# Optimization experiments

Measured on AMD Instinct MI355X. Metric: run time of the kernel, lower is better.

## Reference

```python
import jax, jax.numpy as jnp
import numpy as np

N_NODES = 100_000
N_EDGES = 1_600_000
N_FEAT = 128
N_HID = 64
N_CLASS = 10
N_LAYERS = 3
N_GRAPHS = 1000


def _linear_init(key, fan_in, fan_out):
    kw, kb = jax.random.split(key)
    s = 1.0 / np.sqrt(fan_in)
    w = jax.random.uniform(kw, (fan_in, fan_out), minval=-s, maxval=s, dtype=jnp.float32)
    b = jax.random.uniform(kb, (fan_out,), minval=-s, maxval=s, dtype=jnp.float32)
    return w, b


def setup_inputs() -> dict:
    key = jax.random.key(0)
    ks = jax.random.split(key, 16)
    x = jax.random.normal(ks[0], (N_NODES, N_FEAT), dtype=jnp.float32)
    edge_index = jax.random.randint(ks[1], (2, N_EDGES), 0, N_NODES, dtype=jnp.int64)
    batch = jnp.sort(jax.random.randint(ks[2], (N_NODES,), 0, N_GRAPHS, dtype=jnp.int64))

    pre_w, pre_b = _linear_init(ks[3], N_FEAT, N_HID)
    w1s, b1s, w2s, b2s = [], [], [], []
    for l in range(N_LAYERS):
        w1, b1 = _linear_init(jax.random.fold_in(ks[4], 2 * l), N_HID, N_HID)
        w2, b2 = _linear_init(jax.random.fold_in(ks[4], 2 * l + 1), N_HID, N_HID)
        w1s.append(w1); b1s.append(b1); w2s.append(w2); b2s.append(b2)
    post_w, post_b = _linear_init(ks[5], N_HID, N_HID)
    ro_w, ro_b = _linear_init(ks[6], N_HID, N_CLASS)

    return {
        "x": x, "edge_index": edge_index, "batch": batch,
        "pre_w": pre_w, "pre_b": pre_b,
        "conv_w1": jnp.stack(w1s), "conv_b1": jnp.stack(b1s),
        "conv_w2": jnp.stack(w2s), "conv_b2": jnp.stack(b2s),
        "post_w": post_w, "post_b": post_b,
        "ro_w": ro_w, "ro_b": ro_b,
    }


def reference(x, edge_index, batch, pre_w, pre_b, conv_w1, conv_b1, conv_w2, conv_b2, post_w, post_b, ro_w, ro_b):
    src = edge_index[0]  # message source (x_j)
    dst = edge_index[1]  # message target

    h = x @ pre_w + pre_b  # [N, H]
    for l in range(N_LAYERS):
        # GINConv, eps=0: MLP((1+eps)*h_i + sum_{j in N(i)} h_j)
        agg = jax.ops.segment_sum(h[src], dst, num_segments=N_NODES)
        z = h + agg
        z = jax.nn.relu(z @ conv_w1[l] + conv_b1[l]) @ conv_w2[l] + conv_b2[l]
        h = jax.nn.relu(z)  # dropout is identity in eval mode

    g = jax.ops.segment_sum(h, batch, num_segments=N_GRAPHS)  # global_add_pool [G, H]
    g = jax.nn.relu(g @ post_w + post_b)
    logits = g @ ro_w + ro_b
    return jax.nn.log_softmax(logits, axis=1)
```

## Files before the change

kernel.cpp:

```cpp
#include <hip/hip_runtime.h>
#include <math.h>

#define N_NODES  100000
#define N_FEAT   128
#define N_HID    64
#define N_CLASS  10
#define N_GRAPHS 1000
#define N_EDGES  1600000
#define NTILES   1563
#define BLK_N    128
#define NT2      782
#define HF_PASS  8
#define HF_RANGE 12500
#define CSR_STRIDE 64
#define EMAX_LDS 32

__device__ __forceinline__ float bflo(unsigned u) { return __uint_as_float(u << 16); }
__device__ __forceinline__ float bfhi(unsigned u) { return __uint_as_float(u & 0xffff0000u); }
__device__ __forceinline__ unsigned bf_rne(float f) {
    unsigned u = __float_as_uint(f);
    return (u + 0x7fffu + ((u >> 16) & 1u)) >> 16;
}
__device__ __forceinline__ unsigned pack2(float a, float b) {
    return bf_rne(a) | (bf_rne(b) << 16);
}

__global__ __launch_bounds__(256, 4) void pre_kernel(
    const float* __restrict__ x, const float* __restrict__ W,
    const float* __restrict__ b, uint2* __restrict__ h)
{
    __shared__ float xs[64][68];
    __shared__ float ws[64][68];
    const int tid = threadIdx.x;
    const int tx = tid & 15, ty = tid >> 4;
    const int n0 = blockIdx.x * 64;

    float acc[4][4];
#pragma unroll
    for (int i = 0; i < 4; ++i)
#pragma unroll
        for (int j = 0; j < 4; ++j) acc[i][j] = 0.f;

    for (int p = 0; p < 2; ++p) {
        __syncthreads();
#pragma unroll
        for (int t = 0; t < 4; ++t) {
            const int idx = t * 256 + tid;
            const int m = idx >> 4, kv = idx & 15;
            float4 v = make_float4(0.f, 0.f, 0.f, 0.f);
            if (n0 + m < N_NODES)
                v = *(const float4*)(x + (size_t)(n0 + m) * N_FEAT + p * 64 + kv * 4);
            *(float4*)&xs[m][kv * 4] = v;
            *(float4*)&ws[m][kv * 4] =
                *(const float4*)(W + (size_t)(p * 64 + m) * N_HID + kv * 4);
        }
        __syncthreads();
#pragma unroll 2
        for (int k4 = 0; k4 < 16; ++k4) {
            float4 a[4], bb[4];
#pragma unroll
            for (int i = 0; i < 4; ++i)
                a[i] = *(const float4*)&xs[ty + 16 * i][k4 * 4];
#pragma unroll
            for (int j = 0; j < 4; ++j)
                bb[j] = *(const float4*)&ws[k4 * 4 + j][tx * 4];
#pragma unroll
            for (int i = 0; i < 4; ++i) {
                const float* ap = (const float*)&a[i];
#pragma unroll
                for (int j = 0; j < 4; ++j) {
                    const float* bp = (const float*)&bb[j];
#pragma unroll
                    for (int c = 0; c < 4; ++c)
                        acc[i][c] = fmaf(ap[j], bp[c], acc[i][c]);
                }
            }
        }
    }

    const float4 bias = *(const float4*)(b + tx * 4);
#pragma unroll
    for (int i = 0; i < 4; ++i) {
        const int node = n0 + ty + 16 * i;
        if (node < N_NODES) {
            h[(size_t)node * 16 + tx] = make_uint2(
                pack2(acc[i][0] + bias.x, acc[i][1] + bias.y),
                pack2(acc[i][2] + bias.z, acc[i][3] + bias.w));
        }
    }
}

__global__ __launch_bounds__(256) void hist_fill_kernel(
    const int* __restrict__ ei, int* __restrict__ deg, int* __restrict__ csr)
{
    const int stride = gridDim.x * blockDim.x;
    const int tid0 = blockIdx.x * blockDim.x + threadIdx.x;
    const int4* dst4 = (const int4*)(ei + N_EDGES);
    for (int pass = 0; pass < HF_PASS; ++pass) {
        const int lo = pass * HF_RANGE;
        const int hi = lo + HF_RANGE;
        for (int q = tid0; q < N_EDGES / 4; q += stride) {
            const int4 d = dst4[q];
            const int e0 = q * 4;
            if (d.x >= lo && d.x < hi) {
                int p = atomicAdd(&deg[d.x], 1);
                if (p < CSR_STRIDE) csr[d.x * CSR_STRIDE + p] = ei[e0];
            }
            if (d.y >= lo && d.y < hi) {
                int p = atomicAdd(&deg[d.y], 1);
                if (p < CSR_STRIDE) csr[d.y * CSR_STRIDE + p] = ei[e0 + 1];
            }
            if (d.z >= lo && d.z < hi) {
                int p = atomicAdd(&deg[d.z], 1);
                if (p < CSR_STRIDE) csr[d.z * CSR_STRIDE + p] = ei[e0 + 2];
            }
            if (d.w >= lo && d.w < hi) {
                int p = atomicAdd(&deg[d.w], 1);
                if (p < CSR_STRIDE) csr[d.w * CSR_STRIDE + p] = ei[e0 + 3];
            }
        }
    }
}

__global__ __launch_bounds__(512, 6) void gather_mlp_kernel(
    const uint2* __restrict__ hin, uint2* __restrict__ hout,
    const int* __restrict__ csr, const int* __restrict__ deg,
    const float* __restrict__ W1, const float* __restrict__ b1,
    const float* __restrict__ W2, const float* __restrict__ b2)
{
    __shared__ float as[BLK_N][68];
    __shared__ float ws[64][68];
    __shared__ int   sdeg[BLK_N];
    const int tid = threadIdx.x;
    const int tx = tid & 15, ty = tid >> 4;
    const int sub = tx;
    const int n0 = blockIdx.x * BLK_N;

#pragma unroll
    for (int t = 0; t < 2; ++t) {
        const int idx = t * 512 + tid;
        const int m = idx >> 4, kv = idx & 15;
        *(float4*)&ws[m][kv * 4] = *(const float4*)(W1 + (size_t)m * N_HID + kv * 4);
    }
    if (tid < BLK_N) {
        const int node = n0 + tid;
        sdeg[tid] = (node < N_NODES) ? deg[node] : 0;
    }
#pragma unroll
    for (int t = 0; t < 2; ++t) {
        const int idx = t * 512 + tid;
        const int r = idx >> 3, s4 = idx & 7;
        const int node = n0 + r;
        int4 v = make_int4(0, 0, 0, 0);
        if (node < N_NODES)
            v = *(const int4*)(csr + (size_t)node * CSR_STRIDE + s4 * 4);
        *(int4*)((int*)&as[r][36] + s4 * 4) = v;
    }
    __syncthreads();

    for (int rep = 0; rep < 4; ++rep) {
        const int r = ty + 32 * rep;
        const int node = n0 + r;
        float ax = 0.f, ay = 0.f, az = 0.f, aw = 0.f;
        float bx = 0.f, by = 0.f, bz = 0.f, bw = 0.f;
        if (node < N_NODES) {
            int n = sdeg[r];
            n = n > CSR_STRIDE ? CSR_STRIDE : n;
            const uint2 a0 = hin[(size_t)node * 16 + sub];
            ax = bflo(a0.x); ay = bfhi(a0.x);
            az = bflo(a0.y); aw = bfhi(a0.y);
            const int nn = n > EMAX_LDS ? EMAX_LDS : n;
            const int* eptr = (const int*)&as[r][36];
            if (nn > 0) {
                for (int eb = 0; eb < nn; eb += 8) {
                    uint2 rv[8];
#pragma unroll
                    for (int u = 0; u < 8; ++u) {
                        const int idx = eb + u;
                        const int cl = idx < nn ? idx : nn - 1;
                        rv[u] = hin[(size_t)eptr[cl] * 16 + sub];
                    }
#pragma unroll
                    for (int u = 0; u < 8; u += 2) {
                        if (eb + u < nn) {
                            ax += bflo(rv[u].x); ay += bfhi(rv[u].x);
                            az += bflo(rv[u].y); aw += bfhi(rv[u].y);
                        }
                        if (eb + u + 1 < nn) {
                            bx += bflo(rv[u + 1].x); by += bfhi(rv[u + 1].x);
                            bz += bflo(rv[u + 1].y); bw += bfhi(rv[u + 1].y);
                        }
                    }
                }
            }
            for (int t = EMAX_LDS; t < n; ++t) {
                const int s0 = csr[(size_t)node * CSR_STRIDE + t];
                const uint2 a = hin[(size_t)s0 * 16 + sub];
                ax += bflo(a.x); ay += bfhi(a.x);
                az += bflo(a.y); aw += bfhi(a.y);
            }
        }
        *(float4*)&as[r][sub * 4] =
            make_float4(ax + bx, ay + by, az + bz, aw + bw);
    }
    __syncthreads();

    float acc[4][4];
#pragma unroll
    for (int i = 0; i < 4; ++i)
#pragma unroll
        for (int j = 0; j < 4; ++j) acc[i][j] = 0.f;
#pragma unroll 2
    for (int k4 = 0; k4 < 16; ++k4) {
        float4 a[4], bb[4];
#pragma unroll
        for (int i = 0; i < 4; ++i)
            a[i] = *(const float4*)&as[ty + 32 * i][k4 * 4];
#pragma unroll
        for (int j = 0; j < 4; ++j)
            bb[j] = *(const float4*)&ws[k4 * 4 + j][tx * 4];
#pragma unroll
        for (int i = 0; i < 4; ++i) {
            const float* ap = (const float*)&a[i];
#pragma unroll
            for (int j = 0; j < 4; ++j) {
                const float* bp = (const float*)&bb[j];
#pragma unroll
                for (int c = 0; c < 4; ++c)
                    acc[i][c] = fmaf(ap[j], bp[c], acc[i][c]);
            }
        }
    }
    const float4 bias1 = *(const float4*)(b1 + tx * 4);
    float4 z[4];
#pragma unroll
    for (int i = 0; i < 4; ++i) {
        z[i].x = fmaxf(acc[i][0] + bias1.x, 0.f);
        z[i].y = fmaxf(acc[i][1] + bias1.y, 0.f);
        z[i].z = fmaxf(acc[i][2] + bias1.z, 0.f);
        z[i].w = fmaxf(acc[i][3] + bias1.w, 0.f);
    }
    __syncthreads();
#pragma unroll
    for (int i = 0; i < 4; ++i)
        *(float4*)&as[ty + 32 * i][tx * 4] = z[i];
#pragma unroll
    for (int t = 0; t < 2; ++t) {
        const int idx = t * 512 + tid;
        const int m = idx >> 4, kv = idx & 15;
        *(float4*)&ws[m][kv * 4] = *(const float4*)(W2 + (size_t)m * N_HID + kv * 4);
    }
    __syncthreads();

#pragma unroll
    for (int i = 0; i < 4; ++i)
#pragma unroll
        for (int j = 0; j < 4; ++j) acc[i][j] = 0.f;
#pragma unroll 2
    for (int k4 = 0; k4 < 16; ++k4) {
        float4 a[4], bb[4];
#pragma unroll
        for (int i = 0; i < 4; ++i)
            a[i] = *(const float4*)&as[ty + 32 * i][k4 * 4];
#pragma unroll
        for (int j = 0; j < 4; ++j)
            bb[j] = *(const float4*)&ws[k4 * 4 + j][tx * 4];
#pragma unroll
        for (int i = 0; i < 4; ++i) {
            const float* ap = (const float*)&a[i];
#pragma unroll
            for (int j = 0; j < 4; ++j) {
                const float* bp = (const float*)&bb[j];
#pragma unroll
                for (int c = 0; c < 4; ++c)
                    acc[i][c] = fmaf(ap[j], bp[c], acc[i][c]);
            }
        }
    }
    const float4 bias2 = *(const float4*)(b2 + tx * 4);
#pragma unroll
    for (int i = 0; i < 4; ++i) {
        const int node = n0 + ty + 32 * i;
        if (node < N_NODES) {
            hout[(size_t)node * 16 + tx] = make_uint2(
                pack2(fmaxf(acc[i][0] + bias2.x, 0.f),
                      fmaxf(acc[i][1] + bias2.y, 0.f)),
                pack2(fmaxf(acc[i][2] + bias2.z, 0.f),
                      fmaxf(acc[i][3] + bias2.w, 0.f)));
        }
    }
}

__global__ __launch_bounds__(256) void pool_head_kernel(
    const unsigned short* __restrict__ h, const int* __restrict__ batch,
    const float* __restrict__ Wp, const float* __restrict__ bp,
    const float* __restrict__ Wr, const float* __restrict__ br,
    float* __restrict__ out)
{
    const int graph = blockIdx.x;
    int l = 0, r = N_NODES;
    while (l < r) { int m = (l + r) >> 1; if (batch[m] < graph) l = m + 1; else r = m; }
    const int lo = l;
    r = N_NODES;
    while (l < r) { int m = (l + r) >> 1; if (batch[m] < graph + 1) l = m + 1; else r = m; }
    const int hi = l;

    const int lane = threadIdx.x & 63;
    const int wave = threadIdx.x >> 6;
    float acc = 0.0f;
    for (int i = lo + wave; i < hi; i += 4)
        acc += __uint_as_float(((unsigned)h[(size_t)i * N_HID + lane]) << 16);
    __shared__ float sacc[4][N_HID];
    sacc[wave][lane] = acc;
    __syncthreads();
    if (wave != 0) return;

    const float gv = sacc[0][lane] + sacc[1][lane] + sacc[2][lane] + sacc[3][lane];
    float acc2 = bp[lane];
#pragma unroll
    for (int k = 0; k < N_HID; ++k) {
        const float gk = __int_as_float(
            __builtin_amdgcn_readlane(__float_as_int(gv), k));
        acc2 = fmaf(gk, Wp[k * N_HID + lane], acc2);
    }
    const float y = fmaxf(acc2, 0.f);

    float logit = (lane < N_CLASS) ? br[lane] : 0.f;
#pragma unroll
    for (int k = 0; k < N_HID; ++k) {
        const float yk = __int_as_float(
            __builtin_amdgcn_readlane(__float_as_int(y), k));
        if (lane < N_CLASS)
            logit = fmaf(yk, Wr[k * N_CLASS + lane], logit);
    }

    __shared__ float slog[N_CLASS];
    if (lane < N_CLASS) slog[lane] = logit;
    if (lane < N_CLASS) {
        float m = -INFINITY;
#pragma unroll
        for (int c = 0; c < N_CLASS; ++c) m = fmaxf(m, slog[c]);
        float sum = 0.0f;
#pragma unroll
        for (int c = 0; c < N_CLASS; ++c) sum += expf(slog[c] - m);
        out[(size_t)graph * N_CLASS + lane] = logit - m - logf(sum);
    }
}

extern "C" void kernel_launch(void* const* d_in, const int* in_sizes, int n_in,
                              void* d_out, int out_size, void* d_ws, size_t ws_size,
                              hipStream_t stream)
{
    const float* x       = (const float*)d_in[0];
    const int*   ei      = (const int*)d_in[1];
    const int*   batch   = (const int*)d_in[2];
    const float* pre_w   = (const float*)d_in[3];
    const float* pre_b   = (const float*)d_in[4];
    const float* conv_w1 = (const float*)d_in[5];
    const float* conv_b1 = (const float*)d_in[6];
    const float* conv_w2 = (const float*)d_in[7];
    const float* conv_b2 = (const float*)d_in[8];
    const float* post_w  = (const float*)d_in[9];
    const float* post_b  = (const float*)d_in[10];
    const float* ro_w    = (const float*)d_in[11];
    const float* ro_b    = (const float*)d_in[12];
    float* out = (float*)d_out;

    uint2* h0   = (uint2*)d_ws;
    uint2* h1   = h0 + (size_t)N_NODES * 16;
    int*   deg  = (int*)(h1 + (size_t)N_NODES * 16);
    int*   csr  = deg + N_NODES;

    hipMemsetAsync(deg, 0, N_NODES * sizeof(int), stream);

    pre_kernel<<<NTILES, 256, 0, stream>>>(x, pre_w, pre_b, h0);
    hist_fill_kernel<<<1024, 256, 0, stream>>>(ei, deg, csr);

    gather_mlp_kernel<<<NT2, 512, 0, stream>>>(
        h0, h1, csr, deg,
        conv_w1, conv_b1, conv_w2, conv_b2);
    gather_mlp_kernel<<<NT2, 512, 0, stream>>>(
        h1, h0, csr, deg,
        conv_w1 + N_HID * N_HID, conv_b1 + N_HID,
        conv_w2 + N_HID * N_HID, conv_b2 + N_HID);
    gather_mlp_kernel<<<NT2, 512, 0, stream>>>(
        h0, h1, csr, deg,
        conv_w1 + 2 * N_HID * N_HID, conv_b1 + 2 * N_HID,
        conv_w2 + 2 * N_HID * N_HID, conv_b2 + 2 * N_HID);

    pool_head_kernel<<<N_GRAPHS, 256, 0, stream>>>(
        (const unsigned short*)h1, batch, post_w, post_b, ro_w, ro_b, out);
}
```

Measured before the change: 413.0 us.

## Enlarge pre-projection tiles, unpredicate neighbor gather loop, double histogram grid

The input projection kernel now processes 128 nodes per 512-thread block instead of 64 per 256, so each weight tile load in LDS is shared by more rows, at the cost of more LDS per block. The per-node neighbor gather loop replaces clamped, predicated 8-wide batches with full unpredicated 8-wide batches, then a pairwise tail and a single remainder. This removes redundant clamped loads and per-element branches. The histogram/CSR fill launches twice as many blocks, which may change atomic contention.

```diff
diff --git a/kernel.cpp b/kernel.cpp
--- a/kernel.cpp
+++ b/kernel.cpp
@@ -7,7 +7,6 @@
 #define N_CLASS  10
 #define N_GRAPHS 1000
 #define N_EDGES  1600000
-#define NTILES   1563
 #define BLK_N    128
 #define NT2      782
 #define HF_PASS  8
@@ -25,15 +24,15 @@
     return bf_rne(a) | (bf_rne(b) << 16);
 }
 
-__global__ __launch_bounds__(256, 4) void pre_kernel(
+__global__ __launch_bounds__(512, 6) void pre_kernel(
     const float* __restrict__ x, const float* __restrict__ W,
     const float* __restrict__ b, uint2* __restrict__ h)
 {
-    __shared__ float xs[64][68];
+    __shared__ float xs[BLK_N][68];
     __shared__ float ws[64][68];
     const int tid = threadIdx.x;
     const int tx = tid & 15, ty = tid >> 4;
-    const int n0 = blockIdx.x * 64;
+    const int n0 = blockIdx.x * BLK_N;
 
     float acc[4][4];
 #pragma unroll
@@ -45,12 +44,17 @@
         __syncthreads();
 #pragma unroll
         for (int t = 0; t < 4; ++t) {
-            const int idx = t * 256 + tid;
+            const int idx = t * 512 + tid;
             const int m = idx >> 4, kv = idx & 15;
             float4 v = make_float4(0.f, 0.f, 0.f, 0.f);
             if (n0 + m < N_NODES)
                 v = *(const float4*)(x + (size_t)(n0 + m) * N_FEAT + p * 64 + kv * 4);
             *(float4*)&xs[m][kv * 4] = v;
+        }
+#pragma unroll
+        for (int t = 0; t < 2; ++t) {
+            const int idx = t * 512 + tid;
+            const int m = idx >> 4, kv = idx & 15;
             *(float4*)&ws[m][kv * 4] =
                 *(const float4*)(W + (size_t)(p * 64 + m) * N_HID + kv * 4);
         }
@@ -60,7 +64,7 @@
             float4 a[4], bb[4];
 #pragma unroll
             for (int i = 0; i < 4; ++i)
-                a[i] = *(const float4*)&xs[ty + 16 * i][k4 * 4];
+                a[i] = *(const float4*)&xs[ty + 32 * i][k4 * 4];
 #pragma unroll
             for (int j = 0; j < 4; ++j)
                 bb[j] = *(const float4*)&ws[k4 * 4 + j][tx * 4];
@@ -81,7 +85,7 @@
     const float4 bias = *(const float4*)(b + tx * 4);
 #pragma unroll
     for (int i = 0; i < 4; ++i) {
-        const int node = n0 + ty + 16 * i;
+        const int node = n0 + ty + 32 * i;
         if (node < N_NODES) {
             h[(size_t)node * 16 + tx] = make_uint2(
                 pack2(acc[i][0] + bias.x, acc[i][1] + bias.y),
@@ -171,27 +175,32 @@
             az = bflo(a0.y); aw = bfhi(a0.y);
             const int nn = n > EMAX_LDS ? EMAX_LDS : n;
             const int* eptr = (const int*)&as[r][36];
-            if (nn > 0) {
-                for (int eb = 0; eb < nn; eb += 8) {
-                    uint2 rv[8];
-#pragma unroll
-                    for (int u = 0; u < 8; ++u) {
-                        const int idx = eb + u;
-                        const int cl = idx < nn ? idx : nn - 1;
-                        rv[u] = hin[(size_t)eptr[cl] * 16 + sub];
-                    }
-#pragma unroll
-                    for (int u = 0; u < 8; u += 2) {
-                        if (eb + u < nn) {
-                            ax += bflo(rv[u].x); ay += bfhi(rv[u].x);
-                            az += bflo(rv[u].y); aw += bfhi(rv[u].y);
-                        }
-                        if (eb + u + 1 < nn) {
-                            bx += bflo(rv[u + 1].x); by += bfhi(rv[u + 1].x);
-                            bz += bflo(rv[u + 1].y); bw += bfhi(rv[u + 1].y);
-                        }
-                    }
+            int eb = 0;
+            for (; eb + 8 <= nn; eb += 8) {
+                uint2 rv[8];
+#pragma unroll
+                for (int u = 0; u < 8; ++u)
+                    rv[u] = hin[(size_t)eptr[eb + u] * 16 + sub];
+#pragma unroll
+                for (int u = 0; u < 8; u += 2) {
+                    ax += bflo(rv[u].x);     ay += bfhi(rv[u].x);
+                    az += bflo(rv[u].y);     aw += bfhi(rv[u].y);
+                    bx += bflo(rv[u + 1].x); by += bfhi(rv[u + 1].x);
+                    bz += bflo(rv[u + 1].y); bw += bfhi(rv[u + 1].y);
                 }
+            }
+            for (; eb + 2 <= nn; eb += 2) {
+                const uint2 r0 = hin[(size_t)eptr[eb] * 16 + sub];
+                const uint2 r1 = hin[(size_t)eptr[eb + 1] * 16 + sub];
+                ax += bflo(r0.x); ay += bfhi(r0.x);
+                az += bflo(r0.y); aw += bfhi(r0.y);
+                bx += bflo(r1.x); by += bfhi(r1.x);
+                bz += bflo(r1.y); bw += bfhi(r1.y);
+            }
+            if (eb < nn) {
+                const uint2 r0 = hin[(size_t)eptr[eb] * 16 + sub];
+                ax += bflo(r0.x); ay += bfhi(r0.x);
+                az += bflo(r0.y); aw += bfhi(r0.y);
             }
             for (int t = EMAX_LDS; t < n; ++t) {
                 const int s0 = csr[(size_t)node * CSR_STRIDE + t];
@@ -373,8 +382,8 @@
 
     hipMemsetAsync(deg, 0, N_NODES * sizeof(int), stream);
 
-    pre_kernel<<<NTILES, 256, 0, stream>>>(x, pre_w, pre_b, h0);
-    hist_fill_kernel<<<1024, 256, 0, stream>>>(ei, deg, csr);
+    pre_kernel<<<NT2, 512, 0, stream>>>(x, pre_w, pre_b, h0);
+    hist_fill_kernel<<<2048, 256, 0, stream>>>(ei, deg, csr);
 
     gather_mlp_kernel<<<NT2, 512, 0, stream>>>(
         h0, h1, csr, deg,
```

Measured after the change: 423.8 us. 1.03x slower.
